# Kernel tuning notes

Hardware: AMD Instinct MI355X
Metric: run time of the kernel (lower is better)

The kernel has to match this reference:

```python
import jax, jax.numpy as jnp
import numpy as np

NOISE_DIM = 32
HIDDEN_DIM = 256
DATA_DIM = 2
TEMP = 0.05
N = 16384
DIAG_PENALTY = 1e6


def _cdist(a, b):
    # Euclidean pairwise distance [Na, Nb], safe sqrt (zero grad at d==0 like torch.cdist)
    d2 = (jnp.sum(a * a, -1)[:, None] + jnp.sum(b * b, -1)[None, :]
          - 2.0 * (a @ b.T))
    d2 = jnp.maximum(d2, 0.0)
    safe = jnp.where(d2 > 0, d2, 1.0)
    return jnp.where(d2 > 0, jnp.sqrt(safe), 0.0)


def setup_inputs() -> dict:
    key = jax.random.key(0)
    ks = jax.random.split(key, 12)
    pos = jax.random.normal(ks[0], (N, DATA_DIM), dtype=jnp.float32)
    z = jax.random.normal(ks[1], (N, NOISE_DIM), dtype=jnp.float32)
    def lin(k, fan_in, fan_out):
        bound = 1.0 / np.sqrt(fan_in)
        k1, k2 = jax.random.split(k)
        W = jax.random.uniform(k1, (fan_in, fan_out), minval=-bound, maxval=bound, dtype=jnp.float32)
        b = jax.random.uniform(k2, (fan_out,), minval=-bound, maxval=bound, dtype=jnp.float32)
        return W, b
    W1, b1 = lin(ks[2], NOISE_DIM, HIDDEN_DIM)
    W2, b2 = lin(ks[3], HIDDEN_DIM, HIDDEN_DIM)
    W3, b3 = lin(ks[4], HIDDEN_DIM, HIDDEN_DIM)
    W4, b4 = lin(ks[5], HIDDEN_DIM, HIDDEN_DIM)
    W5, b5 = lin(ks[6], HIDDEN_DIM, DATA_DIM)
    return {"pos": pos, "z": z, "W1": W1, "b1": b1, "W2": W2, "b2": b2,
            "W3": W3, "b3": b3, "W4": W4, "b4": b4, "W5": W5, "b5": b5}


def reference(pos, z, W1, b1, W2, b2, W3, b3, W4, b4, W5, b5):
    # SELU MLP generator
    h = jax.nn.selu(z @ W1 + b1)
    h = jax.nn.selu(h @ W2 + b2)
    h = jax.nn.selu(h @ W3 + b3)
    h = jax.nn.selu(h @ W4 + b4)
    gen = h @ W5 + b5  # [N, D]

    y_pos = jax.lax.stop_gradient(pos)
    y_neg = jax.lax.stop_gradient(gen)

    dist_pos = _cdist(gen, y_pos)  # [N, N]
    dist_neg = _cdist(gen, y_neg)  # [N, N]
    dist_neg = dist_neg + jnp.eye(gen.shape[0], dtype=gen.dtype) * DIAG_PENALTY

    energy_pos = -TEMP * jax.nn.logsumexp(-dist_pos / TEMP, axis=1)
    energy_neg = TEMP * jax.nn.logsumexp(-dist_neg / TEMP, axis=1)
    return energy_pos + energy_neg  # [N]
```

## Files before the change

kernel.cpp:

```cpp
#include <hip/hip_runtime.h>
#include <hip/hip_bf16.h>

#define N_PTS 16384
#define TEMP_F 0.05f

__device__ __forceinline__ float selu_f(float x) {
    const float scale = 1.0507009873554805f;
    const float alpha = 1.6732632423543772f;
    return x > 0.f ? scale * x : scale * alpha * (__expf(x) - 1.f);
}

__device__ __forceinline__ float fast_sqrtf(float x) {
#if __has_builtin(__builtin_amdgcn_sqrtf)
    return __builtin_amdgcn_sqrtf(x);
#else
    return sqrtf(x);
#endif
}

__device__ __forceinline__ float fast_exp2f(float x) {
#if __has_builtin(__builtin_amdgcn_exp2f)
    return __builtin_amdgcn_exp2f(x);
#else
    return exp2f(x);
#endif
}

__device__ __forceinline__ float fast_log2f(float x) {
#if __has_builtin(__builtin_amdgcn_logf)
    return __builtin_amdgcn_logf(x);
#else
    return log2f(x);
#endif
}

__global__ __launch_bounds__(1024) void mlp_kernel(
    const float* __restrict__ z,
    const float* __restrict__ W1, const float* __restrict__ b1,
    const float* __restrict__ W2, const float* __restrict__ b2,
    const float* __restrict__ W3, const float* __restrict__ b3,
    const float* __restrict__ W4, const float* __restrict__ b4,
    const float* __restrict__ W5, const float* __restrict__ b5,
    float* __restrict__ gen)
{
    __shared__ float h[256 * 64];

    const int t = threadIdx.x;
    const int r = t & 63;
    const int w = __builtin_amdgcn_readfirstlane(t >> 6);
    const int c0 = w * 16;
    const int row0 = blockIdx.x * 64;

    #pragma unroll
    for (int e = 0; e < 2; e++) {
        int f  = t + e * 1024;
        int rz = f >> 5;
        int kz = f & 31;
        h[kz * 64 + rz] = z[(row0 + rz) * 32 + kz];
    }
    __syncthreads();

    float acc[16];

    #pragma unroll
    for (int j = 0; j < 16; j++) acc[j] = b1[c0 + j];
    #pragma unroll 8
    for (int k = 0; k < 32; k++) {
        float hv = h[k * 64 + r];
        const float* Wr = W1 + k * 256 + c0;
        #pragma unroll
        for (int j = 0; j < 16; j++) acc[j] = fmaf(hv, Wr[j], acc[j]);
    }
    __syncthreads();
    #pragma unroll
    for (int j = 0; j < 16; j++) h[(c0 + j) * 64 + r] = selu_f(acc[j]);
    __syncthreads();

    for (int layer = 0; layer < 3; layer++) {
        const float* W = (layer == 0) ? W2 : (layer == 1) ? W3 : W4;
        const float* b = (layer == 0) ? b2 : (layer == 1) ? b3 : b4;
        #pragma unroll
        for (int j = 0; j < 16; j++) acc[j] = b[c0 + j];
        #pragma unroll 4
        for (int k = 0; k < 256; k++) {
            float hv = h[k * 64 + r];
            const float* Wr = W + k * 256 + c0;
            #pragma unroll
            for (int j = 0; j < 16; j++) acc[j] = fmaf(hv, Wr[j], acc[j]);
        }
        __syncthreads();
        #pragma unroll
        for (int j = 0; j < 16; j++) h[(c0 + j) * 64 + r] = selu_f(acc[j]);
        __syncthreads();
    }

    float p0 = 0.f, p1 = 0.f;
    #pragma unroll
    for (int kk = 0; kk < 16; kk++) {
        int k = c0 + kk;
        float hv = h[k * 64 + r];
        p0 = fmaf(hv, W5[k * 2 + 0], p0);
        p1 = fmaf(hv, W5[k * 2 + 1], p1);
    }
    __syncthreads();
    h[(0 * 16 + w) * 64 + r] = p0;
    h[(1 * 16 + w) * 64 + r] = p1;
    __syncthreads();
    if (t < 128) {
        int d  = t >> 6;
        int rr = t & 63;
        float sum = b5[d];
        #pragma unroll
        for (int ss = 0; ss < 16; ss++) sum += h[(d * 16 + ss) * 64 + rr];
        gen[(row0 + rr) * 2 + d] = sum;
    }
}

__global__ __launch_bounds__(512) void energy_kernel(
    const float* __restrict__ gen,
    const float* __restrict__ pos,
    float* __restrict__ out)
{
    __shared__ float4 sp[512];
    __shared__ float4 sg[512];

    const int t  = threadIdx.x;
    const int s  = t & 31;
    const int rl = t >> 5;
    const int i  = blockIdx.x * 16 + rl;
    const int diagBase = ((blockIdx.x * 16) >> 10) << 10;

    const float2 q = ((const float2*)gen)[i];

    const float cL2 = 28.853900817779268f;
    const float Tl2 = 0.034657359027997264f;
    const float cB  = 57.707801635558536f;

    float p0 = 0.f, p1 = 0.f, n0 = 0.f, n1 = 0.f;

    for (int base = 0; base < N_PTS; base += 1024) {
        __syncthreads();
        sp[t] = ((const float4*)pos)[base / 2 + t];
        sg[t] = ((const float4*)gen)[base / 2 + t];
        __syncthreads();
        if (base == diagBase) {
            #pragma unroll 4
            for (int u = 0; u < 16; u++) {
                int j = base + 2 * (s + 32 * u);
                float4 pp = sp[s + 32 * u];
                float4 gg = sg[s + 32 * u];
                float dx = q.x - pp.x, dy = q.y - pp.y;
                float d  = fast_sqrtf(fmaf(dx, dx, dy * dy));
                p0 += fast_exp2f(fmaf(-cL2, d, cB));
                dx = q.x - pp.z; dy = q.y - pp.w;
                d  = fast_sqrtf(fmaf(dx, dx, dy * dy));
                p1 += fast_exp2f(fmaf(-cL2, d, cB));
                dx = q.x - gg.x; dy = q.y - gg.y;
                d  = fast_sqrtf(fmaf(dx, dx, dy * dy));
                float e0 = fast_exp2f(fmaf(-cL2, d, cB));
                n0 += (j == i) ? 0.f : e0;
                dx = q.x - gg.z; dy = q.y - gg.w;
                d  = fast_sqrtf(fmaf(dx, dx, dy * dy));
                float e1 = fast_exp2f(fmaf(-cL2, d, cB));
                n1 += (j + 1 == i) ? 0.f : e1;
            }
        } else {
            #pragma unroll 4
            for (int u = 0; u < 16; u++) {
                float4 pp = sp[s + 32 * u];
                float4 gg = sg[s + 32 * u];
                float dx = q.x - pp.x, dy = q.y - pp.y;
                float d  = fast_sqrtf(fmaf(dx, dx, dy * dy));
                p0 += fast_exp2f(fmaf(-cL2, d, cB));
                dx = q.x - pp.z; dy = q.y - pp.w;
                d  = fast_sqrtf(fmaf(dx, dx, dy * dy));
                p1 += fast_exp2f(fmaf(-cL2, d, cB));
                dx = q.x - gg.x; dy = q.y - gg.y;
                d  = fast_sqrtf(fmaf(dx, dx, dy * dy));
                n0 += fast_exp2f(fmaf(-cL2, d, cB));
                dx = q.x - gg.z; dy = q.y - gg.w;
                d  = fast_sqrtf(fmaf(dx, dx, dy * dy));
                n1 += fast_exp2f(fmaf(-cL2, d, cB));
            }
        }
    }

    float sump = p0 + p1;
    float sumn = n0 + n1;
    #pragma unroll
    for (int m = 1; m < 32; m <<= 1) {
        sump += __shfl_xor(sump, m, 32);
        sumn += __shfl_xor(sumn, m, 32);
    }

    if (s == 0) {
        out[i] = Tl2 * (fast_log2f(sumn) - fast_log2f(sump));
    }
}

extern "C" void kernel_launch(void* const* d_in, const int* in_sizes, int n_in,
                              void* d_out, int out_size, void* d_ws, size_t ws_size,
                              hipStream_t stream) {
    const float* pos = (const float*)d_in[0];
    const float* z   = (const float*)d_in[1];
    const float* W1  = (const float*)d_in[2];
    const float* b1  = (const float*)d_in[3];
    const float* W2  = (const float*)d_in[4];
    const float* b2  = (const float*)d_in[5];
    const float* W3  = (const float*)d_in[6];
    const float* b3  = (const float*)d_in[7];
    const float* W4  = (const float*)d_in[8];
    const float* b4  = (const float*)d_in[9];
    const float* W5  = (const float*)d_in[10];
    const float* b5  = (const float*)d_in[11];

    float* gen = (float*)d_ws;

    mlp_kernel<<<N_PTS / 64, 1024, 0, stream>>>(z, W1, b1, W2, b2, W3, b3,
                                                W4, b4, W5, b5, gen);
    energy_kernel<<<N_PTS / 16, 512, 0, stream>>>(gen, pos, (float*)d_out);
}
```

Measured before the change: 292.9 us.

## Register-tile MLP with double-buffered LDS weights; drop LDS staging in energy kernel

The MLP kernel now uses 512 threads, and each thread computes an 8x4 register tile. Weight slabs are staged through double-buffered shared memory, replacing per-thread scalar global weight loads and raising FMA reuse per load. The energy kernel drops its shared-memory staging and block barriers, reads pos/gen directly from global/L2 as float4, and uses smaller 256-thread blocks. This adds more register and LDS pressure in the MLP, and the energy kernel now relies on cache hits instead of explicit sharing.

```diff
diff --git a/kernel.cpp b/kernel.cpp
--- a/kernel.cpp
+++ b/kernel.cpp
@@ -34,7 +34,7 @@
 #endif
 }
 
-__global__ __launch_bounds__(1024) void mlp_kernel(
+__global__ __launch_bounds__(512) void mlp_kernel(
     const float* __restrict__ z,
     const float* __restrict__ W1, const float* __restrict__ b1,
     const float* __restrict__ W2, const float* __restrict__ b2,
@@ -43,92 +43,145 @@
     const float* __restrict__ W5, const float* __restrict__ b5,
     float* __restrict__ gen)
 {
-    __shared__ float h[256 * 64];
-
-    const int t = threadIdx.x;
-    const int r = t & 63;
-    const int w = __builtin_amdgcn_readfirstlane(t >> 6);
-    const int c0 = w * 16;
+    __shared__ float hbuf[256 * 64];
+    __shared__ float wbuf[2][16 * 256];
+
+    const int t  = threadIdx.x;
+    const int l  = t & 63;
+    const int w  = t >> 6;
+    const int r0 = w * 8;
     const int row0 = blockIdx.x * 64;
 
     #pragma unroll
-    for (int e = 0; e < 2; e++) {
-        int f  = t + e * 1024;
+    for (int e = 0; e < 4; e++) {
+        int f  = t + e * 512;
         int rz = f >> 5;
         int kz = f & 31;
-        h[kz * 64 + rz] = z[(row0 + rz) * 32 + kz];
+        hbuf[kz * 64 + rz] = z[(row0 + rz) * 32 + kz];
+    }
+    float* wflat = &wbuf[0][0];
+    #pragma unroll
+    for (int e = 0; e < 4; e++) {
+        int f = t + e * 512;
+        ((float4*)wflat)[f] = ((const float4*)W1)[f];
     }
     __syncthreads();
 
-    float acc[16];
-
-    #pragma unroll
-    for (int j = 0; j < 16; j++) acc[j] = b1[c0 + j];
-    #pragma unroll 8
+    float acc[8][4];
+
+    #pragma unroll
+    for (int g = 0; g < 4; g++) {
+        float bv = b1[l + 64 * g];
+        #pragma unroll
+        for (int i = 0; i < 8; i++) acc[i][g] = bv;
+    }
+    #pragma unroll 4
     for (int k = 0; k < 32; k++) {
-        float hv = h[k * 64 + r];
-        const float* Wr = W1 + k * 256 + c0;
-        #pragma unroll
-        for (int j = 0; j < 16; j++) acc[j] = fmaf(hv, Wr[j], acc[j]);
+        float hv[8], wv[4];
+        *(float4*)&hv[0] = *(const float4*)&hbuf[k * 64 + r0];
+        *(float4*)&hv[4] = *(const float4*)&hbuf[k * 64 + r0 + 4];
+        #pragma unroll
+        for (int g = 0; g < 4; g++) wv[g] = wflat[k * 256 + l + 64 * g];
+        #pragma unroll
+        for (int i = 0; i < 8; i++)
+            #pragma unroll
+            for (int g = 0; g < 4; g++)
+                acc[i][g] = fmaf(hv[i], wv[g], acc[i][g]);
     }
     __syncthreads();
     #pragma unroll
-    for (int j = 0; j < 16; j++) h[(c0 + j) * 64 + r] = selu_f(acc[j]);
+    for (int i = 0; i < 8; i++)
+        #pragma unroll
+        for (int g = 0; g < 4; g++)
+            hbuf[(l + 64 * g) * 64 + r0 + i] = selu_f(acc[i][g]);
     __syncthreads();
 
     for (int layer = 0; layer < 3; layer++) {
         const float* W = (layer == 0) ? W2 : (layer == 1) ? W3 : W4;
         const float* b = (layer == 0) ? b2 : (layer == 1) ? b3 : b4;
         #pragma unroll
-        for (int j = 0; j < 16; j++) acc[j] = b[c0 + j];
+        for (int g = 0; g < 4; g++) {
+            float bv = b[l + 64 * g];
+            #pragma unroll
+            for (int i = 0; i < 8; i++) acc[i][g] = bv;
+        }
+        {
+            float4 a0 = ((const float4*)W)[t];
+            float4 a1 = ((const float4*)W)[t + 512];
+            ((float4*)&wbuf[0][0])[t]       = a0;
+            ((float4*)&wbuf[0][0])[t + 512] = a1;
+        }
+        __syncthreads();
+        for (int s = 0; s < 16; s++) {
+            const int buf = s & 1;
+            float4 nx0, nx1;
+            if (s + 1 < 16) {
+                nx0 = ((const float4*)W)[(s + 1) * 1024 + t];
+                nx1 = ((const float4*)W)[(s + 1) * 1024 + t + 512];
+            }
+            const float* wl = &wbuf[buf][0];
+            #pragma unroll 4
+            for (int kk = 0; kk < 16; kk++) {
+                const int k = s * 16 + kk;
+                float hv[8], wv[4];
+                *(float4*)&hv[0] = *(const float4*)&hbuf[k * 64 + r0];
+                *(float4*)&hv[4] = *(const float4*)&hbuf[k * 64 + r0 + 4];
+                #pragma unroll
+                for (int g = 0; g < 4; g++) wv[g] = wl[kk * 256 + l + 64 * g];
+                #pragma unroll
+                for (int i = 0; i < 8; i++)
+                    #pragma unroll
+                    for (int g = 0; g < 4; g++)
+                        acc[i][g] = fmaf(hv[i], wv[g], acc[i][g]);
+            }
+            if (s + 1 < 16) {
+                ((float4*)&wbuf[1 - buf][0])[t]       = nx0;
+                ((float4*)&wbuf[1 - buf][0])[t + 512] = nx1;
+            }
+            __syncthreads();
+        }
+        #pragma unroll
+        for (int i = 0; i < 8; i++)
+            #pragma unroll
+            for (int g = 0; g < 4; g++)
+                hbuf[(l + 64 * g) * 64 + r0 + i] = selu_f(acc[i][g]);
+        __syncthreads();
+    }
+
+    {
+        const int rr = l;
+        float p0 = 0.f, p1 = 0.f;
         #pragma unroll 4
-        for (int k = 0; k < 256; k++) {
-            float hv = h[k * 64 + r];
-            const float* Wr = W + k * 256 + c0;
-            #pragma unroll
-            for (int j = 0; j < 16; j++) acc[j] = fmaf(hv, Wr[j], acc[j]);
-        }
+        for (int kk = 0; kk < 32; kk++) {
+            int k = w * 32 + kk;
+            float hv = hbuf[k * 64 + rr];
+            p0 = fmaf(hv, W5[2 * k], p0);
+            p1 = fmaf(hv, W5[2 * k + 1], p1);
+        }
+        wbuf[0][w * 64 + rr]       = p0;
+        wbuf[0][512 + w * 64 + rr] = p1;
         __syncthreads();
-        #pragma unroll
-        for (int j = 0; j < 16; j++) h[(c0 + j) * 64 + r] = selu_f(acc[j]);
-        __syncthreads();
-    }
-
-    float p0 = 0.f, p1 = 0.f;
-    #pragma unroll
-    for (int kk = 0; kk < 16; kk++) {
-        int k = c0 + kk;
-        float hv = h[k * 64 + r];
-        p0 = fmaf(hv, W5[k * 2 + 0], p0);
-        p1 = fmaf(hv, W5[k * 2 + 1], p1);
-    }
-    __syncthreads();
-    h[(0 * 16 + w) * 64 + r] = p0;
-    h[(1 * 16 + w) * 64 + r] = p1;
-    __syncthreads();
-    if (t < 128) {
-        int d  = t >> 6;
-        int rr = t & 63;
-        float sum = b5[d];
-        #pragma unroll
-        for (int ss = 0; ss < 16; ss++) sum += h[(d * 16 + ss) * 64 + rr];
-        gen[(row0 + rr) * 2 + d] = sum;
-    }
-}
-
-__global__ __launch_bounds__(512) void energy_kernel(
+        if (t < 128) {
+            int d = t >> 6;
+            int r = t & 63;
+            float sum = b5[d];
+            #pragma unroll
+            for (int ss = 0; ss < 8; ss++) sum += wbuf[0][d * 512 + ss * 64 + r];
+            gen[(row0 + r) * 2 + d] = sum;
+        }
+    }
+}
+
+__global__ __launch_bounds__(256) void energy_kernel(
     const float* __restrict__ gen,
     const float* __restrict__ pos,
     float* __restrict__ out)
 {
-    __shared__ float4 sp[512];
-    __shared__ float4 sg[512];
-
     const int t  = threadIdx.x;
     const int s  = t & 31;
     const int rl = t >> 5;
-    const int i  = blockIdx.x * 16 + rl;
-    const int diagBase = ((blockIdx.x * 16) >> 10) << 10;
+    const int i  = blockIdx.x * 8 + rl;
+    const int diagChunk = (blockIdx.x * 8) >> 10;
 
     const float2 q = ((const float2*)gen)[i];
 
@@ -136,30 +189,31 @@
     const float Tl2 = 0.034657359027997264f;
     const float cB  = 57.707801635558536f;
 
+    const float4* pos4 = (const float4*)pos;
+    const float4* gen4 = (const float4*)gen;
+
     float p0 = 0.f, p1 = 0.f, n0 = 0.f, n1 = 0.f;
 
-    for (int base = 0; base < N_PTS; base += 1024) {
-        __syncthreads();
-        sp[t] = ((const float4*)pos)[base / 2 + t];
-        sg[t] = ((const float4*)gen)[base / 2 + t];
-        __syncthreads();
-        if (base == diagBase) {
+    for (int c = 0; c < 16; c++) {
+        const int base2 = c * 512;
+        if (c == diagChunk) {
             #pragma unroll 4
             for (int u = 0; u < 16; u++) {
-                int j = base + 2 * (s + 32 * u);
-                float4 pp = sp[s + 32 * u];
-                float4 gg = sg[s + 32 * u];
-                float dx = q.x - pp.x, dy = q.y - pp.y;
+                int idx = base2 + s + 32 * u;
+                int j   = idx * 2;
+                float4 P = pos4[idx];
+                float4 G = gen4[idx];
+                float dx = q.x - P.x, dy = q.y - P.y;
                 float d  = fast_sqrtf(fmaf(dx, dx, dy * dy));
                 p0 += fast_exp2f(fmaf(-cL2, d, cB));
-                dx = q.x - pp.z; dy = q.y - pp.w;
+                dx = q.x - P.z; dy = q.y - P.w;
                 d  = fast_sqrtf(fmaf(dx, dx, dy * dy));
                 p1 += fast_exp2f(fmaf(-cL2, d, cB));
-                dx = q.x - gg.x; dy = q.y - gg.y;
+                dx = q.x - G.x; dy = q.y - G.y;
                 d  = fast_sqrtf(fmaf(dx, dx, dy * dy));
                 float e0 = fast_exp2f(fmaf(-cL2, d, cB));
                 n0 += (j == i) ? 0.f : e0;
-                dx = q.x - gg.z; dy = q.y - gg.w;
+                dx = q.x - G.z; dy = q.y - G.w;
                 d  = fast_sqrtf(fmaf(dx, dx, dy * dy));
                 float e1 = fast_exp2f(fmaf(-cL2, d, cB));
                 n1 += (j + 1 == i) ? 0.f : e1;
@@ -167,18 +221,19 @@
         } else {
             #pragma unroll 4
             for (int u = 0; u < 16; u++) {
-                float4 pp = sp[s + 32 * u];
-                float4 gg = sg[s + 32 * u];
-                float dx = q.x - pp.x, dy = q.y - pp.y;
+                int idx = base2 + s + 32 * u;
+                float4 P = pos4[idx];
+                float4 G = gen4[idx];
+                float dx = q.x - P.x, dy = q.y - P.y;
                 float d  = fast_sqrtf(fmaf(dx, dx, dy * dy));
                 p0 += fast_exp2f(fmaf(-cL2, d, cB));
-                dx = q.x - pp.z; dy = q.y - pp.w;
+                dx = q.x - P.z; dy = q.y - P.w;
                 d  = fast_sqrtf(fmaf(dx, dx, dy * dy));
                 p1 += fast_exp2f(fmaf(-cL2, d, cB));
-                dx = q.x - gg.x; dy = q.y - gg.y;
+                dx = q.x - G.x; dy = q.y - G.y;
                 d  = fast_sqrtf(fmaf(dx, dx, dy * dy));
                 n0 += fast_exp2f(fmaf(-cL2, d, cB));
-                dx = q.x - gg.z; dy = q.y - gg.w;
+                dx = q.x - G.z; dy = q.y - G.w;
                 d  = fast_sqrtf(fmaf(dx, dx, dy * dy));
                 n1 += fast_exp2f(fmaf(-cL2, d, cB));
             }
@@ -216,7 +271,7 @@
 
     float* gen = (float*)d_ws;
 
-    mlp_kernel<<<N_PTS / 64, 1024, 0, stream>>>(z, W1, b1, W2, b2, W3, b3,
-                                                W4, b4, W5, b5, gen);
-    energy_kernel<<<N_PTS / 16, 512, 0, stream>>>(gen, pos, (float*)d_out);
-}
+    mlp_kernel<<<N_PTS / 64, 512, 0, stream>>>(z, W1, b1, W2, b2, W3, b3,
+                                               W4, b4, W5, b5, gen);
+    energy_kernel<<<N_PTS / 8, 256, 0, stream>>>(gen, pos, (float*)d_out);
+}
```

Result: slower. 353.1 us (+20.6%).
